# Optimization experiments

Measured on AMD Instinct MI355X. Metric: run time of the kernel, lower is better.

The kernel has to match this reference:

```python
import jax, jax.numpy as jnp
import numpy as np

B, N, D = 8, 2048, 512

def setup_inputs() -> dict:
    key = jax.random.key(0)
    k1, k2, k3, k4 = jax.random.split(key, 4)
    x = jax.random.normal(k1, (B, N, D), dtype=jnp.float32)
    x2 = jax.random.normal(k2, (B, N, D), dtype=jnp.float32)
    # nn.Linear(dim, dim): weight [D, D], bias [D]
    W = jax.random.normal(k3, (D, D), dtype=jnp.float32) * (1.0 / np.sqrt(D))
    b = jax.random.normal(k4, (D,), dtype=jnp.float32) * 0.01
    return {"x": x, "x2": x2, "W": W, "b": b}

def reference(x, x2, W, b):
    # key = softmax(x2.transpose(1,2), dim=1) -> softmax over feature axis D,
    # shape [B, D, N]; equivalently softmax(x2, axis=-1) then transpose.
    key_t = jax.nn.softmax(x2, axis=-1)          # [B, N, D], softmax over D
    query = jax.nn.softmax(x2, axis=1)            # [B, N, D], softmax over N
    # context = value @ key : [B,N,D] @ [B,D,N] -> [B,N,N]
    context = jnp.einsum('bnd,bmd->bnm', x, key_t)
    # atten = context @ query : [B,N,N] @ [B,N,D] -> [B,N,D]
    atten = jnp.einsum('bnm,bmd->bnd', context, query)
    # linear projection: atten @ W.T + b
    return jnp.einsum('bnd,ed->bne', atten, W) + b
```

## Files before the change

### kernel.cpp

```cpp
#include <hip/hip_runtime.h>


typedef __attribute__((ext_vector_type(8))) short          s16x8;
typedef __attribute__((ext_vector_type(8))) unsigned short u16x8;
typedef __attribute__((ext_vector_type(4))) float          f32x4;

#define B_ 8
#define N_ 2048
#define D_ 512

__device__ inline unsigned short f2bf(float f) {
    unsigned u = __float_as_uint(f);
    u += 0x7FFFu + ((u >> 16) & 1u);
    return (unsigned short)(u >> 16);
}

__global__ __launch_bounds__(256) void softmax_fused_k(const float* __restrict__ x2,
                                                       unsigned short* __restrict__ Ft,
                                                       float* __restrict__ qs) {
    __shared__ unsigned short ft[32][522];
    __shared__ float cp[4][512];
    int b = blockIdx.y, m0 = blockIdx.x * 32;
    int w = threadIdx.x >> 6, l = threadIdx.x & 63;
    const int c0 = l * 8;
    float colacc[8] = {0.f, 0.f, 0.f, 0.f, 0.f, 0.f, 0.f, 0.f};
#pragma unroll
    for (int it = 0; it < 8; ++it) {
        int row = w * 8 + it;
        const float* p = x2 + ((size_t)b * N_ + m0 + row) * D_ + c0;
        float4 a = *(const float4*)p;
        float4 bb = *(const float4*)(p + 4);
        float e0 = __expf(a.x), e1 = __expf(a.y), e2 = __expf(a.z), e3 = __expf(a.w);
        float e4 = __expf(bb.x), e5 = __expf(bb.y), e6 = __expf(bb.z), e7 = __expf(bb.w);
        float s = e0 + e1 + e2 + e3 + e4 + e5 + e6 + e7;
#pragma unroll
        for (int off = 1; off < 64; off <<= 1) s += __shfl_xor(s, off);
        float rv = rsqrtf(s);
        u16x8 o;
        o[0] = f2bf(e0 * rv); o[1] = f2bf(e1 * rv); o[2] = f2bf(e2 * rv); o[3] = f2bf(e3 * rv);
        o[4] = f2bf(e4 * rv); o[5] = f2bf(e5 * rv); o[6] = f2bf(e6 * rv); o[7] = f2bf(e7 * rv);
        *(u16x8*)&ft[row][c0] = o;
        colacc[0] += e0; colacc[1] += e1; colacc[2] += e2; colacc[3] += e3;
        colacc[4] += e4; colacc[5] += e5; colacc[6] += e6; colacc[7] += e7;
    }
#pragma unroll
    for (int c = 0; c < 8; ++c) cp[w][c0 + c] = colacc[c];
    __syncthreads();
    for (int c = threadIdx.x; c < 512; c += 256) {
        float s = cp[0][c] + cp[1][c] + cp[2][c] + cp[3][c];
        atomicAdd(&qs[b * D_ + c], s);
    }
    int ml = l & 3, dr = l >> 2;
#pragma unroll
    for (int it = 0; it < 8; ++it) {
        int d = w * 128 + it * 16 + dr;
        u16x8 o;
#pragma unroll
        for (int k = 0; k < 8; ++k) o[k] = ft[ml * 8 + k][d];
        *(u16x8*)(Ft + ((size_t)b * D_ + d) * N_ + m0 + ml * 8) = o;
    }
}

__global__ __launch_bounds__(256) void cvt_bf16_k(const float* __restrict__ in,
                                                  unsigned short* __restrict__ out) {
    size_t i = ((size_t)blockIdx.x * 256 + threadIdx.x) * 8;
    float4 a = *(const float4*)(in + i);
    float4 b = *(const float4*)(in + i + 4);
    u16x8 o;
    o[0] = f2bf(a.x); o[1] = f2bf(a.y); o[2] = f2bf(a.z); o[3] = f2bf(a.w);
    o[4] = f2bf(b.x); o[5] = f2bf(b.y); o[6] = f2bf(b.z); o[7] = f2bf(b.w);
    *(u16x8*)(out + i) = o;
}

__global__ __launch_bounds__(256) void cvt_kq_k(const float* __restrict__ P,
                                                const float* __restrict__ qs,
                                                unsigned short* __restrict__ KQb) {
    size_t o = ((size_t)blockIdx.x * 256 + threadIdx.x) * 8;
    int b = (int)(o >> 18);
    size_t off = o & 262143;
    int j0 = (int)(o & 511);
    const float* base = P + (size_t)b * 4 * 262144 + off;
    float4 s0 = {0.f, 0.f, 0.f, 0.f}, s1 = {0.f, 0.f, 0.f, 0.f};
#pragma unroll
    for (int s = 0; s < 4; ++s) {
        float4 a0 = *(const float4*)(base + (size_t)s * 262144);
        float4 a1 = *(const float4*)(base + (size_t)s * 262144 + 4);
        s0.x += a0.x; s0.y += a0.y; s0.z += a0.z; s0.w += a0.w;
        s1.x += a1.x; s1.y += a1.y; s1.z += a1.z; s1.w += a1.w;
    }
    float4 q0 = *(const float4*)(qs + b * D_ + j0);
    float4 q1 = *(const float4*)(qs + b * D_ + j0 + 4);
    u16x8 r;
    r[0] = f2bf(s0.x / q0.x); r[1] = f2bf(s0.y / q0.y);
    r[2] = f2bf(s0.z / q0.z); r[3] = f2bf(s0.w / q0.w);
    r[4] = f2bf(s1.x / q1.x); r[5] = f2bf(s1.y / q1.y);
    r[6] = f2bf(s1.z / q1.z); r[7] = f2bf(s1.w / q1.w);
    *(u16x8*)(KQb + o) = r;
}

__device__ inline void gload16(const unsigned short* g, unsigned short* l) {
    __builtin_amdgcn_global_load_lds((const __attribute__((address_space(1))) void*)g,
                                     (__attribute__((address_space(3))) void*)l, 16, 0, 0);
}
__device__ inline void gload16f(const float* g, float* l) {
    __builtin_amdgcn_global_load_lds((const __attribute__((address_space(1))) void*)g,
                                     (__attribute__((address_space(3))) void*)l, 16, 0, 0);
}

__global__ __launch_bounds__(256, 2) void gemm128_p2_k(const unsigned short* __restrict__ Ft,
                                                       float* __restrict__ P) {
    __shared__ unsigned short As[128 * 32], Bs[128 * 32];
    const int K = N_;
    int z = blockIdx.z, b = z >> 2, ks = z & 3;
    int k0 = ks * 512;
    const unsigned short* Ab = Ft + (size_t)b * ((size_t)D_ * N_);
    int tid = threadIdx.x, w = tid >> 6, l = tid & 63;
    int wr = w >> 1, wc = w & 1;
    int lr = l & 15, lg = l >> 4;

    f32x4 acc[4][4];
#pragma unroll
    for (int i = 0; i < 4; ++i)
#pragma unroll
        for (int j = 0; j < 4; ++j) acc[i][j] = (f32x4){0.f, 0.f, 0.f, 0.f};

    const int rowbase = blockIdx.y * 128, colbase = blockIdx.x * 128;

    for (int kt = k0; kt < k0 + 512; kt += 32) {
#pragma unroll
        for (int i = 0; i < 2; ++i) {
            int ci = (i * 4 + w) * 64 + l;
            int row = ci >> 2, cc = ci & 3;
            gload16(Ab + (size_t)(rowbase + row) * K + kt + cc * 8, As + (i * 4 + w) * 512);
            gload16(Ab + (size_t)(colbase + row) * K + kt + cc * 8, Bs + (i * 4 + w) * 512);
        }
        __syncthreads();
        s16x8 af[4], bf[4];
#pragma unroll
        for (int i = 0; i < 4; ++i)
            af[i] = *(const s16x8*)&As[(wr * 64 + i * 16 + lr) * 32 + lg * 8];
#pragma unroll
        for (int j = 0; j < 4; ++j)
            bf[j] = *(const s16x8*)&Bs[(wc * 64 + j * 16 + lr) * 32 + lg * 8];
#pragma unroll
        for (int i = 0; i < 4; ++i)
#pragma unroll
            for (int j = 0; j < 4; ++j)
                acc[i][j] = __builtin_amdgcn_mfma_f32_16x16x32_bf16(af[i], bf[j], acc[i][j], 0, 0, 0);
        __syncthreads();
    }

    float* C = P + (size_t)z * 262144;
#pragma unroll
    for (int i = 0; i < 4; ++i)
#pragma unroll
        for (int j = 0; j < 4; ++j) {
            int col = colbase + wc * 64 + j * 16 + lr;
#pragma unroll
            for (int r = 0; r < 4; ++r) {
                int row = rowbase + wr * 64 + i * 16 + lg * 4 + r;
                C[(size_t)row * D_ + col] = acc[i][j][r];
            }
        }
}

__global__ __launch_bounds__(256, 4) void gemm64_k(const unsigned short* __restrict__ A,
                                                   const unsigned short* __restrict__ Bm,
                                                   unsigned short* __restrict__ Cv,
                                                   int K, long long sA, long long sB, long long sC) {
    __shared__ unsigned short As[64 * 32], Bs[64 * 32];
    int b = blockIdx.z;
    const unsigned short* Ab = A + (size_t)b * sA;
    const unsigned short* Bb = Bm + (size_t)b * sB;
    int tid = threadIdx.x, w = tid >> 6, l = tid & 63;
    int wr = w >> 1, wc = w & 1;
    int lr = l & 15, lg = l >> 4;
    int srow = tid >> 2, scc = tid & 3;

    f32x4 acc[2][2];
#pragma unroll
    for (int i = 0; i < 2; ++i)
#pragma unroll
        for (int j = 0; j < 2; ++j) acc[i][j] = (f32x4){0.f, 0.f, 0.f, 0.f};

    const int rowbase = blockIdx.y * 64, colbase = blockIdx.x * 64;

    for (int kt = 0; kt < K; kt += 32) {
        gload16(Ab + (size_t)(rowbase + srow) * K + kt + scc * 8, As + w * 512);
        gload16(Bb + (size_t)(colbase + srow) * K + kt + scc * 8, Bs + w * 512);
        __syncthreads();
        s16x8 af[2], bf[2];
#pragma unroll
        for (int i = 0; i < 2; ++i)
            af[i] = *(const s16x8*)&As[(wr * 32 + i * 16 + lr) * 32 + lg * 8];
#pragma unroll
        for (int j = 0; j < 2; ++j)
            bf[j] = *(const s16x8*)&Bs[(wc * 32 + j * 16 + lr) * 32 + lg * 8];
#pragma unroll
        for (int i = 0; i < 2; ++i)
#pragma unroll
            for (int j = 0; j < 2; ++j)
                acc[i][j] = __builtin_amdgcn_mfma_f32_16x16x32_bf16(af[i], bf[j], acc[i][j], 0, 0, 0);
        __syncthreads();
    }

    unsigned short* C = Cv + (size_t)b * sC;
#pragma unroll
    for (int i = 0; i < 2; ++i)
#pragma unroll
        for (int j = 0; j < 2; ++j) {
            int col = colbase + wc * 32 + j * 16 + lr;
#pragma unroll
            for (int r = 0; r < 4; ++r) {
                int row = rowbase + wr * 32 + i * 16 + lg * 4 + r;
                C[(size_t)row * D_ + col] = f2bf(acc[i][j][r]);
            }
        }
}

__global__ __launch_bounds__(256, 2) void gemm_xf32_k(const float* __restrict__ X,
                                                      const unsigned short* __restrict__ Bm,
                                                      float* __restrict__ Out,
                                                      const float* __restrict__ bias) {
    __shared__ float Asf[128 * 32];
    __shared__ unsigned short Bs[128 * 32];
    int b = blockIdx.z;
    const float* Ab = X + (size_t)b * ((size_t)N_ * D_);
    const unsigned short* Bb = Bm + (size_t)b * ((size_t)D_ * D_);
    int tm = blockIdx.y, tn = blockIdx.x;
    int tid = threadIdx.x, w = tid >> 6, l = tid & 63;
    int wr = w >> 1, wc = w & 1;
    int lr = l & 15, lg = l >> 4;

    f32x4 acc[4][4];
#pragma unroll
    for (int i = 0; i < 4; ++i)
#pragma unroll
        for (int j = 0; j < 4; ++j) acc[i][j] = (f32x4){0.f, 0.f, 0.f, 0.f};

    const int rowbase = tm * 128, colbase = tn * 128;

    for (int kt = 0; kt < D_; kt += 32) {
#pragma unroll
        for (int i = 0; i < 4; ++i) {
            int ci = (i * 4 + w) * 64 + l;
            int row = ci >> 3, cc = ci & 7;
            gload16f(Ab + (size_t)(rowbase + row) * D_ + kt + cc * 4, Asf + (i * 4 + w) * 256);
        }
#pragma unroll
        for (int i = 0; i < 2; ++i) {
            int ci = (i * 4 + w) * 64 + l;
            int row = ci >> 2, cc = ci & 3;
            gload16(Bb + (size_t)(colbase + row) * D_ + kt + cc * 8, Bs + (i * 4 + w) * 512);
        }
        __syncthreads();
        s16x8 af[4], bf[4];
#pragma unroll
        for (int i = 0; i < 4; ++i) {
            const float* ap = &Asf[(wr * 64 + i * 16 + lr) * 32 + lg * 8];
            f32x4 a0 = *(const f32x4*)ap, a1 = *(const f32x4*)(ap + 4);
            s16x8 t;
            t[0] = (short)f2bf(a0[0]); t[1] = (short)f2bf(a0[1]);
            t[2] = (short)f2bf(a0[2]); t[3] = (short)f2bf(a0[3]);
            t[4] = (short)f2bf(a1[0]); t[5] = (short)f2bf(a1[1]);
            t[6] = (short)f2bf(a1[2]); t[7] = (short)f2bf(a1[3]);
            af[i] = t;
        }
#pragma unroll
        for (int j = 0; j < 4; ++j)
            bf[j] = *(const s16x8*)&Bs[(wc * 64 + j * 16 + lr) * 32 + lg * 8];
#pragma unroll
        for (int i = 0; i < 4; ++i)
#pragma unroll
            for (int j = 0; j < 4; ++j)
                acc[i][j] = __builtin_amdgcn_mfma_f32_16x16x32_bf16(af[i], bf[j], acc[i][j], 0, 0, 0);
        __syncthreads();
    }

    float* C = Out + (size_t)b * ((size_t)N_ * D_);
#pragma unroll
    for (int i = 0; i < 4; ++i)
#pragma unroll
        for (int j = 0; j < 4; ++j) {
            int col = colbase + wc * 64 + j * 16 + lr;
            float bv = bias[col];
#pragma unroll
            for (int r = 0; r < 4; ++r) {
                int row = rowbase + wr * 64 + i * 16 + lg * 4 + r;
                C[(size_t)row * D_ + col] = acc[i][j][r] + bv;
            }
        }
}

extern "C" void kernel_launch(void* const* d_in, const int* in_sizes, int n_in,
                              void* d_out, int out_size, void* d_ws, size_t ws_size,
                              hipStream_t stream) {
    const float* x    = (const float*)d_in[0];
    const float* x2   = (const float*)d_in[1];
    const float* W    = (const float*)d_in[2];
    const float* bias = (const float*)d_in[3];
    float* out = (float*)d_out;

    unsigned short* Ft  = (unsigned short*)d_ws;
    unsigned short* Wb  = Ft + 8388608;
    unsigned short* KQb = Wb + 262144;
    unsigned short* Mt  = KQb + 2097152;
    float* P   = (float*)(Mt + 2097152);
    float* qs  = P + 8388608;

    hipMemsetAsync(qs, 0, (size_t)B_ * D_ * sizeof(float), stream);

    softmax_fused_k<<<dim3(N_ / 32, B_), 256, 0, stream>>>(x2, Ft, qs);

    cvt_bf16_k<<<dim3(128), 256, 0, stream>>>(W, Wb);

    gemm128_p2_k<<<dim3(4, 4, B_ * 4), 256, 0, stream>>>(Ft, P);

    cvt_kq_k<<<dim3(1024), 256, 0, stream>>>(P, qs, KQb);

    gemm64_k<<<dim3(8, 8, B_), 256, 0, stream>>>(
        Wb, KQb, Mt, 512, 0LL, (long long)512 * 512, (long long)512 * 512);

    gemm_xf32_k<<<dim3(4, 16, B_), 256, 0, stream>>>(x, Mt, out, bias);
}
```

Measured before the change: 169.6 us.

## Store split-K partials in bf16 and retile final GEMM to full-width rows

The split-K partial products of the F^T·F GEMM are now written as bf16 instead of fp32, which halves the traffic written by that GEMM and read back by the reduce kernel. The reduce kernel unpacks bf16 and sums in fp32. The final x·M GEMM moves from 128x128 tiles to 32-row by 512-column tiles, so each x row is loaded and converted to bf16 only once instead of four times. The cost is that every block now reloads the whole 512x512 M per batch, there are fewer MFMAs per block, and rounding partials to bf16 adds error.

```diff
diff --git a/kernel.cpp b/kernel.cpp
--- a/kernel.cpp
+++ b/kernel.cpp
@@ -13,6 +13,9 @@
     unsigned u = __float_as_uint(f);
     u += 0x7FFFu + ((u >> 16) & 1u);
     return (unsigned short)(u >> 16);
+}
+__device__ inline float bf2f(unsigned short u) {
+    return __uint_as_float((unsigned)u << 16);
 }
 
 __global__ __launch_bounds__(256) void softmax_fused_k(const float* __restrict__ x2,
@@ -72,29 +75,28 @@
     *(u16x8*)(out + i) = o;
 }
 
-__global__ __launch_bounds__(256) void cvt_kq_k(const float* __restrict__ P,
+__global__ __launch_bounds__(256) void cvt_kq_k(const unsigned short* __restrict__ Pbf,
                                                 const float* __restrict__ qs,
                                                 unsigned short* __restrict__ KQb) {
     size_t o = ((size_t)blockIdx.x * 256 + threadIdx.x) * 8;
     int b = (int)(o >> 18);
     size_t off = o & 262143;
     int j0 = (int)(o & 511);
-    const float* base = P + (size_t)b * 4 * 262144 + off;
-    float4 s0 = {0.f, 0.f, 0.f, 0.f}, s1 = {0.f, 0.f, 0.f, 0.f};
+    const unsigned short* base = Pbf + (size_t)b * 4 * 262144 + off;
+    float sm[8] = {0.f, 0.f, 0.f, 0.f, 0.f, 0.f, 0.f, 0.f};
 #pragma unroll
     for (int s = 0; s < 4; ++s) {
-        float4 a0 = *(const float4*)(base + (size_t)s * 262144);
-        float4 a1 = *(const float4*)(base + (size_t)s * 262144 + 4);
-        s0.x += a0.x; s0.y += a0.y; s0.z += a0.z; s0.w += a0.w;
-        s1.x += a1.x; s1.y += a1.y; s1.z += a1.z; s1.w += a1.w;
+        u16x8 v = *(const u16x8*)(base + (size_t)s * 262144);
+#pragma unroll
+        for (int k = 0; k < 8; ++k) sm[k] += bf2f(v[k]);
     }
     float4 q0 = *(const float4*)(qs + b * D_ + j0);
     float4 q1 = *(const float4*)(qs + b * D_ + j0 + 4);
     u16x8 r;
-    r[0] = f2bf(s0.x / q0.x); r[1] = f2bf(s0.y / q0.y);
-    r[2] = f2bf(s0.z / q0.z); r[3] = f2bf(s0.w / q0.w);
-    r[4] = f2bf(s1.x / q1.x); r[5] = f2bf(s1.y / q1.y);
-    r[6] = f2bf(s1.z / q1.z); r[7] = f2bf(s1.w / q1.w);
+    r[0] = f2bf(sm[0] / q0.x); r[1] = f2bf(sm[1] / q0.y);
+    r[2] = f2bf(sm[2] / q0.z); r[3] = f2bf(sm[3] / q0.w);
+    r[4] = f2bf(sm[4] / q1.x); r[5] = f2bf(sm[5] / q1.y);
+    r[6] = f2bf(sm[6] / q1.z); r[7] = f2bf(sm[7] / q1.w);
     *(u16x8*)(KQb + o) = r;
 }
 
@@ -108,7 +110,7 @@
 }
 
 __global__ __launch_bounds__(256, 2) void gemm128_p2_k(const unsigned short* __restrict__ Ft,
-                                                       float* __restrict__ P) {
+                                                       unsigned short* __restrict__ Pbf) {
     __shared__ unsigned short As[128 * 32], Bs[128 * 32];
     const int K = N_;
     int z = blockIdx.z, b = z >> 2, ks = z & 3;
@@ -150,7 +152,7 @@
         __syncthreads();
     }
 
-    float* C = P + (size_t)z * 262144;
+    unsigned short* C = Pbf + (size_t)z * 262144;
 #pragma unroll
     for (int i = 0; i < 4; ++i)
 #pragma unroll
@@ -159,7 +161,7 @@
 #pragma unroll
             for (int r = 0; r < 4; ++r) {
                 int row = rowbase + wr * 64 + i * 16 + lg * 4 + r;
-                C[(size_t)row * D_ + col] = acc[i][j][r];
+                C[(size_t)row * D_ + col] = f2bf(acc[i][j][r]);
             }
         }
 }
@@ -218,46 +220,39 @@
         }
 }
 
-__global__ __launch_bounds__(256, 2) void gemm_xf32_k(const float* __restrict__ X,
+__global__ __launch_bounds__(256, 2) void gemm_x512_k(const float* __restrict__ X,
                                                       const unsigned short* __restrict__ Bm,
                                                       float* __restrict__ Out,
                                                       const float* __restrict__ bias) {
-    __shared__ float Asf[128 * 32];
-    __shared__ unsigned short Bs[128 * 32];
-    int b = blockIdx.z;
+    __shared__ float Asf[32 * 32];
+    __shared__ unsigned short Bs[512 * 32];
+    int b = blockIdx.y;
     const float* Ab = X + (size_t)b * ((size_t)N_ * D_);
     const unsigned short* Bb = Bm + (size_t)b * ((size_t)D_ * D_);
-    int tm = blockIdx.y, tn = blockIdx.x;
     int tid = threadIdx.x, w = tid >> 6, l = tid & 63;
-    int wr = w >> 1, wc = w & 1;
     int lr = l & 15, lg = l >> 4;
 
-    f32x4 acc[4][4];
-#pragma unroll
-    for (int i = 0; i < 4; ++i)
-#pragma unroll
-        for (int j = 0; j < 4; ++j) acc[i][j] = (f32x4){0.f, 0.f, 0.f, 0.f};
-
-    const int rowbase = tm * 128, colbase = tn * 128;
+    f32x4 acc[2][8];
+#pragma unroll
+    for (int i = 0; i < 2; ++i)
+#pragma unroll
+        for (int j = 0; j < 8; ++j) acc[i][j] = (f32x4){0.f, 0.f, 0.f, 0.f};
+
+    const int rowbase = blockIdx.x * 32;
 
     for (int kt = 0; kt < D_; kt += 32) {
-#pragma unroll
-        for (int i = 0; i < 4; ++i) {
-            int ci = (i * 4 + w) * 64 + l;
-            int row = ci >> 3, cc = ci & 7;
-            gload16f(Ab + (size_t)(rowbase + row) * D_ + kt + cc * 4, Asf + (i * 4 + w) * 256);
-        }
+        gload16f(Ab + (size_t)(rowbase + (tid >> 3)) * D_ + kt + (tid & 7) * 4,
+                 Asf + (size_t)tid * 4);
+#pragma unroll
+        for (int i = 0; i < 8; ++i) {
+            int ci = i * 256 + tid;
+            gload16(Bb + (size_t)(ci >> 2) * D_ + kt + (ci & 3) * 8, Bs + (size_t)ci * 8);
+        }
+        __syncthreads();
+        s16x8 af[2], bf[8];
 #pragma unroll
         for (int i = 0; i < 2; ++i) {
-            int ci = (i * 4 + w) * 64 + l;
-            int row = ci >> 2, cc = ci & 3;
-            gload16(Bb + (size_t)(colbase + row) * D_ + kt + cc * 8, Bs + (i * 4 + w) * 512);
-        }
-        __syncthreads();
-        s16x8 af[4], bf[4];
-#pragma unroll
-        for (int i = 0; i < 4; ++i) {
-            const float* ap = &Asf[(wr * 64 + i * 16 + lr) * 32 + lg * 8];
+            const float* ap = &Asf[(i * 16 + lr) * 32 + lg * 8];
             f32x4 a0 = *(const f32x4*)ap, a1 = *(const f32x4*)(ap + 4);
             s16x8 t;
             t[0] = (short)f2bf(a0[0]); t[1] = (short)f2bf(a0[1]);
@@ -267,26 +262,26 @@
             af[i] = t;
         }
 #pragma unroll
-        for (int j = 0; j < 4; ++j)
-            bf[j] = *(const s16x8*)&Bs[(wc * 64 + j * 16 + lr) * 32 + lg * 8];
-#pragma unroll
-        for (int i = 0; i < 4; ++i)
-#pragma unroll
-            for (int j = 0; j < 4; ++j)
+        for (int j = 0; j < 8; ++j)
+            bf[j] = *(const s16x8*)&Bs[(w * 128 + j * 16 + lr) * 32 + lg * 8];
+#pragma unroll
+        for (int i = 0; i < 2; ++i)
+#pragma unroll
+            for (int j = 0; j < 8; ++j)
                 acc[i][j] = __builtin_amdgcn_mfma_f32_16x16x32_bf16(af[i], bf[j], acc[i][j], 0, 0, 0);
         __syncthreads();
     }
 
     float* C = Out + (size_t)b * ((size_t)N_ * D_);
 #pragma unroll
-    for (int i = 0; i < 4; ++i)
-#pragma unroll
-        for (int j = 0; j < 4; ++j) {
-            int col = colbase + wc * 64 + j * 16 + lr;
+    for (int i = 0; i < 2; ++i)
+#pragma unroll
+        for (int j = 0; j < 8; ++j) {
+            int col = w * 128 + j * 16 + lr;
             float bv = bias[col];
 #pragma unroll
             for (int r = 0; r < 4; ++r) {
-                int row = rowbase + wr * 64 + i * 16 + lg * 4 + r;
+                int row = rowbase + i * 16 + lg * 4 + r;
                 C[(size_t)row * D_ + col] = acc[i][j][r] + bv;
             }
         }
@@ -305,8 +300,8 @@
     unsigned short* Wb  = Ft + 8388608;
     unsigned short* KQb = Wb + 262144;
     unsigned short* Mt  = KQb + 2097152;
-    float* P   = (float*)(Mt + 2097152);
-    float* qs  = P + 8388608;
+    unsigned short* Pbf = Mt + 2097152;
+    float* qs = (float*)(Pbf + 8388608);
 
     hipMemsetAsync(qs, 0, (size_t)B_ * D_ * sizeof(float), stream);
 
@@ -314,12 +309,12 @@
 
     cvt_bf16_k<<<dim3(128), 256, 0, stream>>>(W, Wb);
 
-    gemm128_p2_k<<<dim3(4, 4, B_ * 4), 256, 0, stream>>>(Ft, P);
-
-    cvt_kq_k<<<dim3(1024), 256, 0, stream>>>(P, qs, KQb);
+    gemm128_p2_k<<<dim3(4, 4, B_ * 4), 256, 0, stream>>>(Ft, Pbf);
+
+    cvt_kq_k<<<dim3(1024), 256, 0, stream>>>(Pbf, qs, KQb);
 
     gemm64_k<<<dim3(8, 8, B_), 256, 0, stream>>>(
         Wb, KQb, Mt, 512, 0LL, (long long)512 * 512, (long long)512 * 512);
 
-    gemm_xf32_k<<<dim3(4, 16, B_), 256, 0, stream>>>(x, Mt, out, bias);
-}
+    gemm_x512_k<<<dim3(N_ / 32, B_), 256, 0, stream>>>(x, Mt, out, bias);
+}
```

Measured after the change: 174.5 us. 2.8% more time.
